# Optimization experiments

Hardware: AMD Instinct MI355X
Metric: run time of the kernel (lower is better)

Reference implementation:

```python
import jax, jax.numpy as jnp
import numpy as np

B, H, V, W = 64, 4, 128000, 200  # batch, heads, vocab, repetition window
N = B * H
NEG = jnp.float32(-1e30)


def setup_inputs() -> dict:
    key = jax.random.key(0)
    ks = jax.random.split(key, 6)
    logits = jax.random.normal(ks[0], (B, H, V), jnp.float32) * 4.0
    output_tokens = jax.random.randint(ks[1], (N, W), 0, V)  # pad value would be V
    temperatures = jax.random.uniform(ks[2], (N,), jnp.float32, 0.5, 1.5)
    top_ps = jax.random.uniform(ks[3], (N,), jnp.float32, 0.7, 1.0)
    top_ks = jax.random.randint(ks[4], (N,), 1, 1025).astype(jnp.int32)
    repetition_penalties = jax.random.uniform(ks[5], (N,), jnp.float32, 1.0, 1.3)
    return {
        "logits": logits,
        "output_tokens": output_tokens,
        "temperatures": temperatures,
        "top_ps": top_ps,
        "top_ks": top_ks,
        "repetition_penalties": repetition_penalties,
    }


def reference(logits, output_tokens, temperatures, top_ps, top_ks, repetition_penalties):
    b, h, v = logits.shape
    n = b * h
    lg = logits.reshape(n, v)

    # --- repetition penalty (bincount-based mask, pad id = v is dropped) ---
    rows = jnp.arange(n)[:, None]
    counts = jnp.zeros((n, v + 1), jnp.int32).at[rows, output_tokens].add(1)[:, :v]
    seen = counts > 0
    rp = jnp.where(seen, repetition_penalties[:, None], 1.0)
    lg = jnp.where(lg > 0, lg / rp, lg * rp)

    # --- temperature ---
    lg = lg / temperatures[:, None]

    # --- top-k / top-p (vLLM: ascending sort, mask, scatter back) ---
    idx = jnp.argsort(lg, axis=-1)                       # ascending
    ls = jnp.take_along_axis(lg, idx, axis=-1)
    kth = jnp.take_along_axis(ls, (v - top_ks.astype(jnp.int32))[:, None], axis=-1)
    ls = jnp.where(ls < kth, NEG, ls)                    # top-k mask
    ps = jax.nn.softmax(ls, axis=-1)
    csum = jnp.cumsum(ps, axis=-1)
    pmask = (csum <= 1.0 - top_ps[:, None]).at[:, -1].set(False)
    ls = jnp.where(pmask, NEG, ls)                       # top-p mask
    inv = jnp.argsort(idx, axis=-1)                      # scatter back
    lg = jnp.take_along_axis(ls, inv, axis=-1)

    # --- softmax + multinomial sample (categorical == multinomial(probs, 1)) ---
    probs = jax.nn.softmax(lg, axis=-1)
    ids = jax.random.categorical(jax.random.key(42), lg, axis=-1).reshape(b, h)
    return ids, probs
```

## Files before the change

### kernel.cpp

```cpp
#include <hip/hip_runtime.h>

#define V 128000
#define V4 (V / 4)
#define V4ALL (NROWS * V4)
#define NCHUNK (V / 16)
#define NROWS 256
#define NSLICE 8
#define SL4 (V4 / NSLICE)
#define W 200
#define VW (V / 32)
#define CAP 4096
#define CAPS 2048
#define CAPM 8192
#define TINYF 1.17549435e-38f
#define HIDX(b) ((b) + ((b) >> 5))
#define HSZ 4224

#define WS_CMAX   0u
#define WS_BMAX   4104192u
#define WS_NEED   16777216u

typedef float vfloat4 __attribute__((ext_vector_type(4)));

__device__ __forceinline__ void bar_lds() {
  asm volatile("s_waitcnt lgkmcnt(0)" ::: "memory");
  __builtin_amdgcn_s_barrier();
}

__device__ __forceinline__ unsigned int fkey(float x) {
  unsigned int u = __float_as_uint(x);
  return (u & 0x80000000u) ? ~u : (u | 0x80000000u);
}
__device__ __forceinline__ float ikey(unsigned int k) {
  unsigned int u = (k & 0x80000000u) ? (k & 0x7FFFFFFFu) : ~k;
  return __uint_as_float(u);
}

__device__ __forceinline__ unsigned int tf_bits(unsigned int t) {
  const unsigned int k0 = 0u, k1 = 42u;
  const unsigned int ks2 = k0 ^ k1 ^ 0x1BD11BDAu;
  unsigned int x0 = 0u + k0, x1 = t + k1;
  const unsigned int ksArr[3] = {k0, k1, ks2};
  const int RA[4] = {13, 15, 26, 6};
  const int RB[4] = {17, 29, 16, 24};
#pragma unroll
  for (int i = 0; i < 5; ++i) {
#pragma unroll
    for (int j = 0; j < 4; ++j) {
      int r = (i & 1) ? RB[j] : RA[j];
      x0 += x1;
      x1 = (x1 << r) | (x1 >> (32 - r));
      x1 ^= x0;
    }
    x0 += ksArr[(i + 1) % 3];
    x1 += ksArr[(i + 2) % 3] + (unsigned int)(i + 1);
  }
  return x0 ^ x1;
}

__device__ __forceinline__ float xform(float x, bool seen, float rp, float irp,
                                        float itemp) {
  if (seen) x = (x > 0.0f) ? x * irp : x * rp;
  return x * itemp;
}

__device__ __forceinline__ void wave_suffix_select_p(const int* hist, int need,
                                                     int lane, int* out_b,
                                                     int* out_rem) {
  int sm = 0;
  const int bb = lane * 64;
  for (int i = 0; i < 64; ++i) sm += hist[HIDX(bb + i)];
  int sfx = sm;
#pragma unroll
  for (int d = 1; d < 64; d <<= 1) {
    int t = __shfl_down(sfx, d);
    if (lane + d < 64) sfx += t;
  }
  unsigned long long mk = __ballot(sfx >= need);
  const int cstar = 63 - __builtin_clzll(mk);
  const int aboveC = __shfl(sfx, cstar) - __shfl(sm, cstar);
  int h = hist[HIDX(cstar * 64 + lane)];
  int sfx2 = h;
#pragma unroll
  for (int d = 1; d < 64; d <<= 1) {
    int t = __shfl_down(sfx2, d);
    if (lane + d < 64) sfx2 += t;
  }
  unsigned long long mk2 = __ballot(aboveC + sfx2 >= need);
  const int boff = 63 - __builtin_clzll(mk2);
  const int aboveB = aboveC + __shfl(sfx2, boff) - __shfl(h, boff);
  if (lane == 0) {
    *out_b = cstar * 64 + boff;
    *out_rem = need - aboveB;
  }
}

__global__ __launch_bounds__(256) void kF_zero(float* __restrict__ probs) {
  vfloat4* __restrict__ p4 = reinterpret_cast<vfloat4*>(probs);
  const vfloat4 z4 = (vfloat4){0.0f, 0.0f, 0.0f, 0.0f};
  const int stride = gridDim.x * 256;
  for (int q = blockIdx.x * 256 + threadIdx.x; q < V4ALL; q += stride)
    p4[q] = z4;
}

__global__ __launch_bounds__(256) void kA_chunkmax(
    const float* __restrict__ logits, const int* __restrict__ toks,
    const float* __restrict__ temps, const float* __restrict__ rps,
    unsigned short* __restrict__ ws_cmax, float* __restrict__ ws_bmax) {
  __shared__ unsigned int s_seen[VW];
  __shared__ float s_red[4];
  const int row = blockIdx.x >> 3;
  const int slice = blockIdx.x & 7;
  const int tid = threadIdx.x;
  const int lane = tid & 63;
  const int wid = tid >> 6;
  const float rp = rps[row];
  const float irp = 1.0f / rp;
  const float itemp = 1.0f / temps[row];
  const size_t base = (size_t)row * V;
  const float4* __restrict__ lg4 = reinterpret_cast<const float4*>(logits + base);

  for (int i = tid; i < VW; i += 256) s_seen[i] = 0u;
  __syncthreads();
  for (int i = tid; i < W; i += 256) {
    int tok = toks[row * W + i];
    if (tok >= 0 && tok < V) atomicOr(&s_seen[tok >> 5], 1u << (tok & 31));
  }
  __syncthreads();

  float lmax = -INFINITY;
  const int q0 = slice * SL4;
  for (int qi = tid; qi < SL4; qi += 256) {
    const int q = q0 + qi;
    float4 x4 = lg4[q];
    float xs[4] = {x4.x, x4.y, x4.z, x4.w};
    const int j0 = q * 4;
    const int sh = j0 & 31;
    unsigned long long ww = (unsigned long long)s_seen[j0 >> 5] |
                            ((unsigned long long)s_seen[(j0 + 3) >> 5] << 32);
    unsigned int kmax = 0u;
#pragma unroll
    for (int e = 0; e < 4; ++e) {
      float x = xform(xs[e], (ww >> (sh + e)) & 1ull, rp, irp, itemp);
      lmax = fmaxf(lmax, x);
      unsigned int ky = fkey(x);
      kmax = kmax > ky ? kmax : ky;
    }
    unsigned int o;
    o = __shfl_xor(kmax, 1); kmax = kmax > o ? kmax : o;
    o = __shfl_xor(kmax, 2); kmax = kmax > o ? kmax : o;
    if ((lane & 3) == 0) ws_cmax[row * NCHUNK + (q >> 2)] = (unsigned short)(kmax >> 16);
  }
#pragma unroll
  for (int d = 32; d > 0; d >>= 1) lmax = fmaxf(lmax, __shfl_xor(lmax, d));
  if (lane == 0) s_red[wid] = lmax;
  __syncthreads();
  if (tid == 0) {
    float mm = fmaxf(fmaxf(s_red[0], s_red[1]), fmaxf(s_red[2], s_red[3]));
    ws_bmax[row * NSLICE + slice] = mm;
  }
}

__global__ __launch_bounds__(1024) void kB_select(
    const float* __restrict__ logits, const int* __restrict__ toks,
    const float* __restrict__ temps, const float* __restrict__ topps,
    const int* __restrict__ topks, const float* __restrict__ rps,
    const unsigned short* __restrict__ ws_cmax, const float* __restrict__ ws_bmax,
    float* __restrict__ out_ids, float* __restrict__ probs) {
  __shared__ unsigned long long s_key[CAP];
  __shared__ __align__(16) unsigned char s_bufA[HSZ*4];
  __shared__ __align__(16) unsigned char s_bufB[16384];
  __shared__ float s_wredf[16];
  __shared__ int s_wredi[16];
  __shared__ float s_mv, s_dn1, s_dn2;
  __shared__ int s_b0, s_cnt, s_scnt, s_selb, s_selrem, s_p0v, s_maxpop;

  int* s_hist0 = (int*)s_key;
  unsigned int* s_seen = (unsigned int*)s_bufA;
  int* s_hist = (int*)s_bufA;
  unsigned short* s_cmax16 = (unsigned short*)s_bufB;
  unsigned long long* s_key2 = (unsigned long long*)s_bufB;
  unsigned long long* s_skey = s_key;
  float* s_e2 = (float*)(s_key + CAPS);
  float* s_q2 = (float*)(s_key + CAPS + CAPS / 2);
  unsigned char* s_keep = (unsigned char*)s_bufA;

  const int row = blockIdx.x;
  const int tid = threadIdx.x;
  const int lane = tid & 63;
  const int wid = tid >> 6;
  const float rp = rps[row];
  const float irp = 1.0f / rp;
  const float itemp = 1.0f / temps[row];
  const float topp = topps[row];
  const int k = topks[row];
  const size_t base = (size_t)row * V;
  const float4* __restrict__ lg4 = reinterpret_cast<const float4*>(logits + base);
  float* __restrict__ prow = probs + base;

  for (int i = tid; i < VW; i += 1024) s_seen[i] = 0u;
  for (int i = tid; i < HSZ; i += 1024) s_hist0[i] = 0;
  {
    const unsigned int* cm32 = reinterpret_cast<const unsigned int*>(ws_cmax + row * NCHUNK);
    unsigned int* sc32 = reinterpret_cast<unsigned int*>(s_cmax16);
    for (int i = tid; i < NCHUNK / 2; i += 1024) sc32[i] = cm32[i];
  }
  __syncthreads();
  for (int i = tid; i < W; i += 1024) {
    int tok = toks[row * W + i];
    if (tok >= 0 && tok < V) atomicOr(&s_seen[tok >> 5], 1u << (tok & 31));
  }
  for (int i = tid; i < NCHUNK; i += 1024)
    atomicAdd(&s_hist0[HIDX(s_cmax16[i] >> 4)], 1);
  __syncthreads();

  if (wid == 1 && lane == 0) {
    float mm = ws_bmax[row * NSLICE];
    for (int i = 1; i < NSLICE; ++i) mm = fmaxf(mm, ws_bmax[row * NSLICE + i]);
    s_mv = mm;
  }
  if (wid == 0) {
    wave_suffix_select_p(s_hist0, k, lane, &s_b0, &s_selrem);
    if (lane == 0) s_cnt = 0;
  }
  __syncthreads();
  const int b0 = s_b0;

  const unsigned int fk0 = ((unsigned int)b0) << 20;
  const int c16 = b0 << 4;
  for (int qb = 0; qb < V4; qb += 1024) {
    const int q = qb + tid;
    const bool act = (q < V4) && ((int)s_cmax16[q >> 2] >= c16);
    unsigned int ks[4];
    bool pr[4] = {false, false, false, false};
    const int j0 = q * 4;
    if (act) {
      float4 x4 = lg4[q];
      float raw[4] = {x4.x, x4.y, x4.z, x4.w};
      const int sh = j0 & 31;
      unsigned long long ww = (unsigned long long)s_seen[j0 >> 5] |
                              ((unsigned long long)s_seen[(j0 + 3) >> 5] << 32);
#pragma unroll
      for (int e = 0; e < 4; ++e) {
        float x = xform(raw[e], (ww >> (sh + e)) & 1ull, rp, irp, itemp);
        ks[e] = fkey(x);
        pr[e] = (ks[e] >= fk0);
      }
    }
    int cnt = (int)pr[0] + (int)pr[1] + (int)pr[2] + (int)pr[3];
    int inc = cnt;
#pragma unroll
    for (int d = 1; d < 64; d <<= 1) {
      int t = __shfl_up(inc, d);
      if (lane >= d) inc += t;
    }
    const int total = __shfl(inc, 63);
    if (total) {
      int basep = 0;
      if (lane == 0) basep = atomicAdd(&s_cnt, total);
      basep = __shfl(basep, 0);
      int off = basep + inc - cnt;
#pragma unroll
      for (int e = 0; e < 4; ++e) {
        if (pr[e]) {
          if (off < CAP)
            s_key[off] = ((unsigned long long)ks[e] << 32) | (unsigned int)(j0 + e);
          ++off;
        }
      }
    }
  }
  bar_lds();
  int G = s_cnt;
  if (G > CAP) G = CAP;
  const int kk = k > G ? G : k;

  for (int i = tid; i < HSZ; i += 1024) s_hist[i] = 0;
  bar_lds();
  for (int i = tid; i < G; i += 1024)
    atomicAdd(&s_hist[HIDX((unsigned int)(s_key[i] >> 52))], 1);
  bar_lds();
  if (wid == 0) {
    wave_suffix_select_p(s_hist, kk, lane, &s_selb, &s_selrem);
    if (lane == 0) s_scnt = 0;
  }
  bar_lds();
  const unsigned int b1 = (unsigned int)s_selb;

  for (int ib = 0; ib < G; ib += 1024) {
    const int i = ib + tid;
    const bool p = (i < G) && ((unsigned int)(s_key[i] >> 52) >= b1);
    unsigned long long mask = __ballot(p);
    if (!mask) continue;
    int basep = 0;
    if (lane == 0) basep = atomicAdd(&s_scnt, __popcll(mask));
    basep = __shfl(basep, 0);
    if (p) {
      int pos = basep + __popcll(mask & ((1ull << lane) - 1ull));
      if (pos < CAPS) s_key2[pos] = s_key[i];
    }
  }
  bar_lds();
  int S = s_scnt;
  if (S > CAPS) S = CAPS;
  const float m = s_mv;

  const unsigned int cbase = b1 << 20;
  const unsigned int span = fkey(m) - cbase;
  int shiftb;
  {
    int bits = 32 - __clz((int)(span | 1u));
    shiftb = bits > 12 ? bits - 12 : 0;
  }
  for (int i = tid; i < HSZ; i += 1024) s_hist[i] = 0;
  bar_lds();
  for (int i = tid; i < S; i += 1024) {
    unsigned int hi = (unsigned int)(s_key2[i] >> 32);
    int b = (int)((hi - cbase) >> shiftb);
    if (b > 4095) b = 4095;
    atomicAdd(&s_hist[HIDX(b)], 1);
  }
  bar_lds();
  if (wid == 0) {
    int T = 0, mx = 0;
    const int bb = lane * 64;
    for (int i = 0; i < 64; ++i) {
      int c = s_hist[HIDX(bb + i)];
      T += c;
      mx = c > mx ? c : mx;
    }
    int ex = T;
#pragma unroll
    for (int d = 1; d < 64; d <<= 1) {
      int t = __shfl_up(ex, d);
      if (lane >= d) ex += t;
    }
    ex -= T;
    int run = ex;
    for (int i = 0; i < 64; ++i) {
      int idx = HIDX(bb + i);
      int c = s_hist[idx];
      s_hist[idx] = run;
      run += c;
    }
#pragma unroll
    for (int d = 32; d > 0; d >>= 1) {
      int o = __shfl_xor(mx, d);
      mx = o > mx ? o : mx;
    }
    if (lane == 0) s_maxpop = mx;
  }
  bar_lds();

  if (s_maxpop <= 16) {
    for (int i = tid; i < S; i += 1024) {
      unsigned long long key = s_key2[i];
      unsigned int hi = (unsigned int)(key >> 32);
      int b = (int)((hi - cbase) >> shiftb);
      if (b > 4095) b = 4095;
      int pos = atomicAdd(&s_hist[HIDX(b)], 1);
      s_skey[pos] = key;
    }
    bar_lds();
    for (int b = tid; b < 4096; b += 1024) {
      int endb = s_hist[HIDX(b)];
      int st = (b == 0) ? 0 : s_hist[HIDX(b - 1)];
      for (int i = st + 1; i < endb; ++i) {
        unsigned long long key = s_skey[i];
        int j = i - 1;
        while (j >= st && s_skey[j] > key) {
          s_skey[j + 1] = s_skey[j];
          --j;
        }
        s_skey[j + 1] = key;
      }
    }
    bar_lds();
  } else {
    int np2 = 2;
    while (np2 < S) np2 <<= 1;
    for (int i = S + tid; i < np2; i += 1024) s_key2[i] = ~0ull;
    bar_lds();
    for (int size = 2; size <= np2; size <<= 1) {
      for (int stride = size >> 1; stride > 0; stride >>= 1) {
        for (int t2 = tid; t2 < (np2 >> 1); t2 += 1024) {
          int pos = 2 * t2 - (t2 & (stride - 1));
          int qq = pos + stride;
          bool up = ((pos & size) == 0);
          unsigned long long a = s_key2[pos], b = s_key2[qq];
          if ((a > b) == up) { s_key2[pos] = b; s_key2[qq] = a; }
        }
        bar_lds();
      }
    }
    for (int i = tid; i < S; i += 1024) s_skey[i] = s_key2[i];
    bar_lds();
  }

  const unsigned int kthkey32 = (unsigned int)(s_skey[S - kk] >> 32);
  for (int i = tid; i < S; i += 1024) {
    unsigned int hi = (unsigned int)(s_skey[i] >> 32);
    if (hi >= kthkey32 && (i == 0 || (unsigned int)(s_skey[i - 1] >> 32) < kthkey32))
      s_p0v = i;
  }
  bar_lds();
  const int p0 = s_p0v;
  const int L = S - p0;

  float part = 0.0f;
  for (int i = tid; i < L; i += 1024) {
    float x = ikey((unsigned int)(s_skey[p0 + i] >> 32));
    float e = expf(x - m);
    s_e2[i] = e;
    part += e;
  }
#pragma unroll
  for (int d = 32; d > 0; d >>= 1) part += __shfl_xor(part, d);
  if (lane == 0) s_wredf[wid] = part;
  bar_lds();
  if (tid == 0) {
    float s = 0.0f;
    for (int i = 0; i < 16; ++i) s += s_wredf[i];
    s_dn1 = s;
  }
  bar_lds();
  const float denom = s_dn1;

  for (int i = tid; i < L; i += 1024) s_q2[i] = s_e2[i] / denom;
  bar_lds();

  if (tid == 0) {
    const float cut = 1.0f - topp;
    float cs = 0.0f;
    int i = 0;
    for (; i + 16 <= L; i += 16) {
      vfloat4 a = *(const vfloat4*)&s_q2[i];
      vfloat4 b = *(const vfloat4*)&s_q2[i + 4];
      vfloat4 c = *(const vfloat4*)&s_q2[i + 8];
      vfloat4 d = *(const vfloat4*)&s_q2[i + 12];
      unsigned int w0, w1, w2, w3;
      cs += a.x; w0  = (cs <= cut) ? 0u : 1u;
      cs += a.y; w0 |= ((cs <= cut) ? 0u : 1u) << 8;
      cs += a.z; w0 |= ((cs <= cut) ? 0u : 1u) << 16;
      cs += a.w; w0 |= ((cs <= cut) ? 0u : 1u) << 24;
      cs += b.x; w1  = (cs <= cut) ? 0u : 1u;
      cs += b.y; w1 |= ((cs <= cut) ? 0u : 1u) << 8;
      cs += b.z; w1 |= ((cs <= cut) ? 0u : 1u) << 16;
      cs += b.w; w1 |= ((cs <= cut) ? 0u : 1u) << 24;
      cs += c.x; w2  = (cs <= cut) ? 0u : 1u;
      cs += c.y; w2 |= ((cs <= cut) ? 0u : 1u) << 8;
      cs += c.z; w2 |= ((cs <= cut) ? 0u : 1u) << 16;
      cs += c.w; w2 |= ((cs <= cut) ? 0u : 1u) << 24;
      cs += d.x; w3  = (cs <= cut) ? 0u : 1u;
      cs += d.y; w3 |= ((cs <= cut) ? 0u : 1u) << 8;
      cs += d.z; w3 |= ((cs <= cut) ? 0u : 1u) << 16;
      cs += d.w; w3 |= ((cs <= cut) ? 0u : 1u) << 24;
      *(unsigned int*)&s_keep[i] = w0;
      *(unsigned int*)&s_keep[i + 4] = w1;
      *(unsigned int*)&s_keep[i + 8] = w2;
      *(unsigned int*)&s_keep[i + 12] = w3;
    }
    for (; i < L; ++i) {
      cs += s_q2[i];
      s_keep[i] = (cs <= cut) ? 0 : 1;
    }
    s_keep[L - 1] = 1;
  }
  bar_lds();

  part = 0.0f;
  for (int i = tid; i < L; i += 1024)
    if (s_keep[i]) part += s_e2[i];
#pragma unroll
  for (int d = 32; d > 0; d >>= 1) part += __shfl_xor(part, d);
  if (lane == 0) s_wredf[wid] = part;
  bar_lds();
  if (tid == 0) {
    float s = 0.0f;
    for (int i = 0; i < 16; ++i) s += s_wredf[i];
    s_dn2 = s;
  }
  bar_lds();
  const float denom2 = s_dn2;

  for (int i = tid; i < L; i += 1024)
    s_e2[i] = s_keep[i] ? (s_e2[i] / denom2) : 0.0f;
  bar_lds();

  float bs = -INFINITY;
  int bi = 0x7FFFFFFF;
  for (int i = tid; i < L; i += 1024) {
    if (!s_keep[i]) continue;
    unsigned long long kv = s_skey[p0 + i];
    int j = (int)(kv & 0xFFFFFFFFull);
    float x = ikey((unsigned int)(kv >> 32));
    unsigned int t = (unsigned int)(row * V) + (unsigned int)j;
    unsigned int bb = tf_bits(t);
    float u = __uint_as_float((bb >> 9) | 0x3f800000u) - 1.0f;
    if (u < TINYF) u = TINYF;
    float g = -logf(-logf(u));
    float sc = x + g;
    if (sc > bs || (sc == bs && j < bi)) { bs = sc; bi = j; }
  }

  for (int i = tid; i < L; i += 1024) {
    int j = (int)(s_skey[p0 + i] & 0xFFFFFFFFull);
    prow[j] = s_e2[i];
  }

#pragma unroll
  for (int d = 32; d > 0; d >>= 1) {
    float ov = __shfl_down(bs, d);
    int oi = __shfl_down(bi, d);
    if (ov > bs || (ov == bs && oi < bi)) { bs = ov; bi = oi; }
  }
  if (lane == 0) { s_wredf[wid] = bs; s_wredi[wid] = bi; }
  bar_lds();
  if (tid == 0) {
    float bb = s_wredf[0];
    int bj = s_wredi[0];
    for (int i = 1; i < 16; ++i) {
      if (s_wredf[i] > bb || (s_wredf[i] == bb && s_wredi[i] < bj)) {
        bb = s_wredf[i];
        bj = s_wredi[i];
      }
    }
    out_ids[row] = (float)bj;
  }
}

__global__ __launch_bounds__(1024, 1) void sampler_mono(
    const float* __restrict__ logits, const int* __restrict__ toks,
    const float* __restrict__ temps, const float* __restrict__ topps,
    const int* __restrict__ topks, const float* __restrict__ rps,
    float* __restrict__ out_ids, float* __restrict__ probs) {
  __shared__ unsigned int s_seen[VW];
  __shared__ int s_hist[4096];
  __shared__ unsigned short s_cmax16[NCHUNK];
  __shared__ float s_sval[CAPM];
  __shared__ int s_sidx[CAPM];
  __shared__ float s_e[CAPM];
  __shared__ unsigned char s_keep[CAPM];
  __shared__ float s_wredf[16];
  __shared__ int s_wredi[16];
  __shared__ float s_m, s_denom, s_denom2;
  __shared__ int s_b0, s_cnt, s_p0;

  const int row = blockIdx.x;
  const int tid = threadIdx.x;
  const int lane = tid & 63;
  const int wid = tid >> 6;
  const float rp = rps[row];
  const float irp = 1.0f / rp;
  const float itemp = 1.0f / temps[row];
  const float topp = topps[row];
  const int k = topks[row];
  const size_t base = (size_t)row * V;
  const float4* __restrict__ lg4 = reinterpret_cast<const float4*>(logits + base);
  vfloat4* __restrict__ pr4 = reinterpret_cast<vfloat4*>(probs + base);

  for (int i = tid; i < VW; i += 1024) s_seen[i] = 0u;
  for (int i = tid; i < 4096; i += 1024) s_hist[i] = 0;
  __syncthreads();
  for (int i = tid; i < W; i += 1024) {
    int tok = toks[row * W + i];
    if (tok >= 0 && tok < V) atomicOr(&s_seen[tok >> 5], 1u << (tok & 31));
  }
  __syncthreads();

  float lmax = -INFINITY;
  for (int qb = 0; qb < V4; qb += 1024) {
    const int q = qb + tid;
    unsigned int kmax = 0u;
    if (q < V4) {
      float4 x4 = lg4[q];
      float xs[4] = {x4.x, x4.y, x4.z, x4.w};
      const int j0 = q * 4;
      const int sh = j0 & 31;
      unsigned long long ww = (unsigned long long)s_seen[j0 >> 5] |
                              ((unsigned long long)s_seen[(j0 + 3) >> 5] << 32);
#pragma unroll
      for (int e = 0; e < 4; ++e) {
        float x = xform(xs[e], (ww >> (sh + e)) & 1ull, rp, irp, itemp);
        lmax = fmaxf(lmax, x);
        unsigned int ky = fkey(x);
        kmax = kmax > ky ? kmax : ky;
      }
    }
    unsigned int o;
    o = __shfl_xor(kmax, 1); kmax = kmax > o ? kmax : o;
    o = __shfl_xor(kmax, 2); kmax = kmax > o ? kmax : o;
    if (((lane & 3) == 0) && (q < V4)) s_cmax16[q >> 2] = (unsigned short)(kmax >> 16);
  }
#pragma unroll
  for (int d = 32; d > 0; d >>= 1) lmax = fmaxf(lmax, __shfl_xor(lmax, d));
  if (lane == 0) s_wredf[wid] = lmax;
  __syncthreads();
  for (int i = tid; i < NCHUNK; i += 1024)
    atomicAdd(&s_hist[s_cmax16[i] >> 4], 1);
  __syncthreads();
  if (wid == 1 && lane == 0) {
    float mm = s_wredf[0];
    for (int i = 1; i < 16; ++i) mm = fmaxf(mm, s_wredf[i]);
    s_m = mm;
  }
  if (wid == 0) {
    int sm = 0;
    const int bb = lane * 64;
    for (int i = 0; i < 64; ++i) sm += s_hist[bb + i];
    int sfx = sm;
#pragma unroll
    for (int d = 1; d < 64; d <<= 1) {
      int t = __shfl_down(sfx, d);
      if (lane + d < 64) sfx += t;
    }
    unsigned long long mk = __ballot(sfx >= k);
    const int cstar = 63 - __builtin_clzll(mk);
    const int above = __shfl(sfx, cstar) - __shfl(sm, cstar);
    int h = s_hist[cstar * 64 + lane];
    int sfx2 = h;
#pragma unroll
    for (int d = 1; d < 64; d <<= 1) {
      int t = __shfl_down(sfx2, d);
      if (lane + d < 64) sfx2 += t;
    }
    unsigned long long mk2 = __ballot(above + sfx2 >= k);
    const int boff = 63 - __builtin_clzll(mk2);
    if (lane == 0) { s_b0 = cstar * 64 + boff; s_cnt = 0; }
  }
  __syncthreads();
  const int b0 = s_b0;
  const unsigned int fk0 = ((unsigned int)b0) << 20;
  const int c16 = b0 << 4;
  for (int qb = 0; qb < V4; qb += 1024) {
    const int q = qb + tid;
    const bool act = (q < V4) && ((int)s_cmax16[q >> 2] >= c16);
    float xs[4];
    bool pr[4] = {false, false, false, false};
    const int j0 = q * 4;
    if (act) {
      float4 x4 = lg4[q];
      float raw[4] = {x4.x, x4.y, x4.z, x4.w};
      const int sh = j0 & 31;
      unsigned long long ww = (unsigned long long)s_seen[j0 >> 5] |
                              ((unsigned long long)s_seen[(j0 + 3) >> 5] << 32);
#pragma unroll
      for (int e = 0; e < 4; ++e) {
        xs[e] = xform(raw[e], (ww >> (sh + e)) & 1ull, rp, irp, itemp);
        pr[e] = (fkey(xs[e]) >= fk0);
      }
    }
#pragma unroll
    for (int e = 0; e < 4; ++e) {
      unsigned long long mask = __ballot(pr[e]);
      if (!mask) continue;
      int basep = 0;
      if (lane == 0) basep = atomicAdd(&s_cnt, __popcll(mask));
      basep = __shfl(basep, 0);
      if (pr[e]) {
        int pos = basep + __popcll(mask & ((1ull << lane) - 1ull));
        if (pos < CAPM) { s_sval[pos] = xs[e]; s_sidx[pos] = j0 + e; }
      }
    }
  }
  __syncthreads();
  int G = s_cnt;
  if (G > CAPM) G = CAPM;
  int np2 = 2;
  while (np2 < G) np2 <<= 1;
  for (int i = G + tid; i < np2; i += 1024) {
    s_sval[i] = INFINITY;
    s_sidx[i] = 0x7FFFFFFF;
  }
  __syncthreads();
  for (int size = 2; size <= np2; size <<= 1) {
    for (int stride = size >> 1; stride > 0; stride >>= 1) {
      for (int t2 = tid; t2 < (np2 >> 1); t2 += 1024) {
        int pos = 2 * t2 - (t2 & (stride - 1));
        int qq = pos + stride;
        bool up = ((pos & size) == 0);
        float v1 = s_sval[pos], v2 = s_sval[qq];
        int i1 = s_sidx[pos], i2 = s_sidx[qq];
        bool gt = (v1 > v2) || (v1 == v2 && i1 > i2);
        if (gt == up) {
          s_sval[pos] = v2; s_sval[qq] = v1;
          s_sidx[pos] = i2; s_sidx[qq] = i1;
        }
      }
      __syncthreads();
    }
  }
  const int kk = k > G ? G : k;
  const float kth = s_sval[G - kk];
  const float m = s_m;
  for (int i = tid; i < G; i += 1024) {
    if (s_sval[i] >= kth && (i == 0 || s_sval[i - 1] < kth)) s_p0 = i;
  }
  __syncthreads();
  const int p0 = s_p0;
  float part = 0.0f;
  for (int i = p0 + tid; i < G; i += 1024) {
    float e = expf(s_sval[i] - m);
    s_e[i] = e;
    part += e;
  }
#pragma unroll
  for (int d = 32; d > 0; d >>= 1) part += __shfl_xor(part, d);
  if (lane == 0) s_wredf[wid] = part;
  __syncthreads();
  if (tid == 0) {
    float s = 0.0f;
    for (int i = 0; i < 16; ++i) s += s_wredf[i];
    s_denom = s;
  }
  __syncthreads();
  const float denom = s_denom;
  if (tid == 0) {
    const float cut = 1.0f - topp;
    float cs = 0.0f;
    for (int i = p0; i < G; ++i) {
      cs += s_e[i] / denom;
      s_keep[i] = (cs <= cut) ? 0 : 1;
    }
    s_keep[G - 1] = 1;
  }
  __syncthreads();
  part = 0.0f;
  for (int i = p0 + tid; i < G; i += 1024)
    if (s_keep[i]) part += s_e[i];
#pragma unroll
  for (int d = 32; d > 0; d >>= 1) part += __shfl_xor(part, d);
  if (lane == 0) s_wredf[wid] = part;
  __syncthreads();
  if (tid == 0) {
    float s = 0.0f;
    for (int i = 0; i < 16; ++i) s += s_wredf[i];
    s_denom2 = s;
  }
  __syncthreads();
  const float denom2 = s_denom2;
  for (int i = p0 + tid; i < G; i += 1024)
    s_e[i] = s_keep[i] ? (s_e[i] / denom2) : 0.0f;
  __syncthreads();
  float bs = -INFINITY;
  int bi = 0x7FFFFFFF;
  for (int i = p0 + tid; i < G; i += 1024) {
    if (!s_keep[i]) continue;
    int j = s_sidx[i];
    unsigned int t = (unsigned int)(row * V) + (unsigned int)j;
    unsigned int bb = tf_bits(t);
    float u = __uint_as_float((bb >> 9) | 0x3f800000u) - 1.0f;
    if (u < TINYF) u = TINYF;
    float g = -logf(-logf(u));
    float sc = s_sval[i] + g;
    if (sc > bs || (sc == bs && j < bi)) { bs = sc; bi = j; }
  }
  const unsigned int kkey = fkey(kth);
  const int k16 = (int)(kkey >> 16);
  for (int q = tid; q < V4; q += 1024) {
    vfloat4 o = (vfloat4){0.0f, 0.0f, 0.0f, 0.0f};
    if ((int)s_cmax16[q >> 2] >= k16) {
      float4 x4 = lg4[q];
      float raw[4] = {x4.x, x4.y, x4.z, x4.w};
      float os[4];
      const int j0 = q * 4;
      const int sh = j0 & 31;
      unsigned long long ww = (unsigned long long)s_seen[j0 >> 5] |
                              ((unsigned long long)s_seen[(j0 + 3) >> 5] << 32);
#pragma unroll
      for (int e = 0; e < 4; ++e) {
        float x = xform(raw[e], (ww >> (sh + e)) & 1ull, rp, irp, itemp);
        float pr = 0.0f;
        if (x >= kth) {
          int j = j0 + e;
          int lo = p0, hi = G;
          while (lo < hi) {
            int mid = (lo + hi) >> 1;
            float v = s_sval[mid];
            int id = s_sidx[mid];
            if (v < x || (v == x && id < j)) lo = mid + 1; else hi = mid;
          }
          pr = s_e[lo];
        }
        os[e] = pr;
      }
      o.x = os[0]; o.y = os[1]; o.z = os[2]; o.w = os[3];
    }
    pr4[q] = o;
  }
#pragma unroll
  for (int d = 32; d > 0; d >>= 1) {
    float ov = __shfl_down(bs, d);
    int oi = __shfl_down(bi, d);
    if (ov > bs || (ov == bs && oi < bi)) { bs = ov; bi = oi; }
  }
  if (lane == 0) { s_wredf[wid] = bs; s_wredi[wid] = bi; }
  __syncthreads();
  if (tid == 0) {
    float bb = s_wredf[0];
    int bj = s_wredi[0];
    for (int i = 1; i < 16; ++i) {
      if (s_wredf[i] > bb || (s_wredf[i] == bb && s_wredi[i] < bj)) {
        bb = s_wredf[i];
        bj = s_wredi[i];
      }
    }
    out_ids[row] = (float)bj;
  }
}

extern "C" void kernel_launch(void* const* d_in, const int* in_sizes, int n_in,
                              void* d_out, int out_size, void* d_ws, size_t ws_size,
                              hipStream_t stream) {
  (void)in_sizes; (void)out_size;
  if (n_in < 6) return;
  const float* logits = (const float*)d_in[0];
  const int* toks = (const int*)d_in[1];
  const float* temps = (const float*)d_in[2];
  const float* topps = (const float*)d_in[3];
  const int* topks = (const int*)d_in[4];
  const float* rps = (const float*)d_in[5];
  float* out = (float*)d_out;
  float* probs = out + NROWS;

  if (ws_size >= WS_NEED && d_ws != nullptr) {
    char* w = (char*)d_ws;
    unsigned short* ws_cmax = (unsigned short*)(w + WS_CMAX);
    float* ws_bmax = (float*)(w + WS_BMAX);
    kF_zero<<<dim3(2048), dim3(256), 0, stream>>>(probs);
    kA_chunkmax<<<dim3(NROWS * NSLICE), dim3(256), 0, stream>>>(
        logits, toks, temps, rps, ws_cmax, ws_bmax);
    kB_select<<<dim3(NROWS), dim3(1024), 0, stream>>>(
        logits, toks, temps, topps, topks, rps, ws_cmax, ws_bmax, out, probs);
  } else {
    sampler_mono<<<dim3(NROWS), dim3(1024), 0, stream>>>(
        logits, toks, temps, topps, topks, rps, out, probs);
  }
}
```

Baseline: 119.7 us.

## Split select kernel into threshold, sliced gather, and finish kernels

Breaks the per-row 1024-thread select kernel into three kernels. A small kernel computes the coarse threshold bucket from the chunk maxima. A gather kernel with 8 blocks per row then scans logit slices in parallel and appends candidate keys to global workspace through a global atomic counter. A finish kernel loads those keys and runs the remaining selection and sampling. Histograms are also replicated four ways in LDS to reduce atomic contention. The aim is more parallelism in the logit-scanning pass, at the cost of extra launches and global round-trips for keys and counters.

```diff
diff --git a/kernel.cpp b/kernel.cpp
--- a/kernel.cpp
+++ b/kernel.cpp
@@ -2,11 +2,12 @@
 
 #define V 128000
 #define V4 (V / 4)
+#define NROWS 256
 #define V4ALL (NROWS * V4)
 #define NCHUNK (V / 16)
-#define NROWS 256
 #define NSLICE 8
 #define SL4 (V4 / NSLICE)
+#define SLC (NCHUNK / NSLICE)
 #define W 200
 #define VW (V / 32)
 #define CAP 4096
@@ -18,6 +19,9 @@
 
 #define WS_CMAX   0u
 #define WS_BMAX   4104192u
+#define WS_B0     4112384u
+#define WS_CNT    4113408u
+#define WS_KEYS   8388608u
 #define WS_NEED   16777216u
 
 typedef float vfloat4 __attribute__((ext_vector_type(4)));
@@ -161,79 +165,73 @@
   }
 }
 
-__global__ __launch_bounds__(1024) void kB_select(
-    const float* __restrict__ logits, const int* __restrict__ toks,
-    const float* __restrict__ temps, const float* __restrict__ topps,
-    const int* __restrict__ topks, const float* __restrict__ rps,
-    const unsigned short* __restrict__ ws_cmax, const float* __restrict__ ws_bmax,
-    float* __restrict__ out_ids, float* __restrict__ probs) {
-  __shared__ unsigned long long s_key[CAP];
-  __shared__ __align__(16) unsigned char s_bufA[HSZ*4];
-  __shared__ __align__(16) unsigned char s_bufB[16384];
-  __shared__ float s_wredf[16];
-  __shared__ int s_wredi[16];
-  __shared__ float s_mv, s_dn1, s_dn2;
-  __shared__ int s_b0, s_cnt, s_scnt, s_selb, s_selrem, s_p0v, s_maxpop;
-
-  int* s_hist0 = (int*)s_key;
-  unsigned int* s_seen = (unsigned int*)s_bufA;
-  int* s_hist = (int*)s_bufA;
-  unsigned short* s_cmax16 = (unsigned short*)s_bufB;
-  unsigned long long* s_key2 = (unsigned long long*)s_bufB;
-  unsigned long long* s_skey = s_key;
-  float* s_e2 = (float*)(s_key + CAPS);
-  float* s_q2 = (float*)(s_key + CAPS + CAPS / 2);
-  unsigned char* s_keep = (unsigned char*)s_bufA;
-
+__global__ __launch_bounds__(1024) void kS_b0(
+    const unsigned short* __restrict__ ws_cmax, const int* __restrict__ topks,
+    int* __restrict__ ws_b0, int* __restrict__ ws_cnt) {
+  __shared__ int s_h[4 * HSZ];
+  __shared__ int s_b, s_rem;
   const int row = blockIdx.x;
   const int tid = threadIdx.x;
   const int lane = tid & 63;
   const int wid = tid >> 6;
+  for (int i = tid; i < 4 * HSZ; i += 1024) s_h[i] = 0;
+  __syncthreads();
+  const unsigned short* cm = ws_cmax + row * NCHUNK;
+  const int rep = (tid & 3) * HSZ;
+  for (int i = tid; i < NCHUNK; i += 1024)
+    atomicAdd(&s_h[rep + HIDX(cm[i] >> 4)], 1);
+  __syncthreads();
+  for (int i = tid; i < HSZ; i += 1024)
+    s_h[i] += s_h[i + HSZ] + s_h[i + 2 * HSZ] + s_h[i + 3 * HSZ];
+  __syncthreads();
+  if (wid == 0) wave_suffix_select_p(s_h, topks[row], lane, &s_b, &s_rem);
+  __syncthreads();
+  if (tid == 0) {
+    ws_b0[row] = s_b;
+    ws_cnt[row] = 0;
+  }
+}
+
+__global__ __launch_bounds__(256) void kB1_gather(
+    const float* __restrict__ logits, const int* __restrict__ toks,
+    const float* __restrict__ temps, const float* __restrict__ rps,
+    const unsigned short* __restrict__ ws_cmax, const int* __restrict__ ws_b0,
+    int* __restrict__ ws_cnt, unsigned long long* __restrict__ ws_keys) {
+  __shared__ unsigned int s_seen[VW];
+  __shared__ unsigned short s_cm[SLC];
+  const int row = blockIdx.x >> 3;
+  const int slice = blockIdx.x & 7;
+  const int tid = threadIdx.x;
+  const int lane = tid & 63;
   const float rp = rps[row];
   const float irp = 1.0f / rp;
   const float itemp = 1.0f / temps[row];
-  const float topp = topps[row];
-  const int k = topks[row];
   const size_t base = (size_t)row * V;
   const float4* __restrict__ lg4 = reinterpret_cast<const float4*>(logits + base);
-  float* __restrict__ prow = probs + base;
-
-  for (int i = tid; i < VW; i += 1024) s_seen[i] = 0u;
-  for (int i = tid; i < HSZ; i += 1024) s_hist0[i] = 0;
-  {
-    const unsigned int* cm32 = reinterpret_cast<const unsigned int*>(ws_cmax + row * NCHUNK);
-    unsigned int* sc32 = reinterpret_cast<unsigned int*>(s_cmax16);
-    for (int i = tid; i < NCHUNK / 2; i += 1024) sc32[i] = cm32[i];
-  }
-  __syncthreads();
-  for (int i = tid; i < W; i += 1024) {
+
+  for (int i = tid; i < VW; i += 256) s_seen[i] = 0u;
+  for (int i = tid; i < SLC; i += 256)
+    s_cm[i] = ws_cmax[row * NCHUNK + slice * SLC + i];
+  __syncthreads();
+  for (int i = tid; i < W; i += 256) {
     int tok = toks[row * W + i];
     if (tok >= 0 && tok < V) atomicOr(&s_seen[tok >> 5], 1u << (tok & 31));
   }
-  for (int i = tid; i < NCHUNK; i += 1024)
-    atomicAdd(&s_hist0[HIDX(s_cmax16[i] >> 4)], 1);
-  __syncthreads();
-
-  if (wid == 1 && lane == 0) {
-    float mm = ws_bmax[row * NSLICE];
-    for (int i = 1; i < NSLICE; ++i) mm = fmaxf(mm, ws_bmax[row * NSLICE + i]);
-    s_mv = mm;
-  }
-  if (wid == 0) {
-    wave_suffix_select_p(s_hist0, k, lane, &s_b0, &s_selrem);
-    if (lane == 0) s_cnt = 0;
-  }
-  __syncthreads();
-  const int b0 = s_b0;
-
+  __syncthreads();
+
+  const int b0 = ws_b0[row];
   const unsigned int fk0 = ((unsigned int)b0) << 20;
   const int c16 = b0 << 4;
-  for (int qb = 0; qb < V4; qb += 1024) {
-    const int q = qb + tid;
-    const bool act = (q < V4) && ((int)s_cmax16[q >> 2] >= c16);
+  unsigned long long* __restrict__ krow = ws_keys + (size_t)row * CAP;
+  const int q0 = slice * SL4;
+  for (int qb = 0; qb < SL4; qb += 256) {
+    const int qi = qb + tid;
+    const bool inb = (qi < SL4);
+    const bool act = inb && ((int)s_cm[qi >> 2] >= c16);
+    const int q = q0 + qi;
+    const int j0 = q * 4;
     unsigned int ks[4];
     bool pr[4] = {false, false, false, false};
-    const int j0 = q * 4;
     if (act) {
       float4 x4 = lg4[q];
       float raw[4] = {x4.x, x4.y, x4.z, x4.w};
@@ -257,31 +255,72 @@
     const int total = __shfl(inc, 63);
     if (total) {
       int basep = 0;
-      if (lane == 0) basep = atomicAdd(&s_cnt, total);
+      if (lane == 0) basep = atomicAdd(&ws_cnt[row], total);
       basep = __shfl(basep, 0);
       int off = basep + inc - cnt;
 #pragma unroll
       for (int e = 0; e < 4; ++e) {
         if (pr[e]) {
           if (off < CAP)
-            s_key[off] = ((unsigned long long)ks[e] << 32) | (unsigned int)(j0 + e);
+            krow[off] = ((unsigned long long)ks[e] << 32) | (unsigned int)(j0 + e);
           ++off;
         }
       }
     }
   }
-  bar_lds();
-  int G = s_cnt;
+}
+
+__global__ __launch_bounds__(1024) void kB2_finish(
+    const float* __restrict__ topps, const int* __restrict__ topks,
+    const float* __restrict__ ws_bmax, const int* __restrict__ ws_cnt,
+    const unsigned long long* __restrict__ ws_keys,
+    float* __restrict__ out_ids, float* __restrict__ probs) {
+  __shared__ unsigned long long s_key[CAP];
+  __shared__ __align__(16) int s_h[4 * HSZ];
+  __shared__ __align__(16) unsigned char s_bufB[16384];
+  __shared__ float s_wredf[16];
+  __shared__ int s_wredi[16];
+  __shared__ float s_mv, s_dn1, s_dn2;
+  __shared__ int s_scnt, s_selb, s_selrem, s_p0v, s_maxpop;
+
+  unsigned long long* s_key2 = (unsigned long long*)s_bufB;
+  unsigned long long* s_skey = s_key;
+  float* s_e2 = (float*)(s_key + CAPS);
+  float* s_q2 = (float*)(s_key + CAPS + CAPS / 2);
+  unsigned char* s_keep = (unsigned char*)s_h;
+
+  const int row = blockIdx.x;
+  const int tid = threadIdx.x;
+  const int lane = tid & 63;
+  const int wid = tid >> 6;
+  const float topp = topps[row];
+  const int k = topks[row];
+  float* __restrict__ prow = probs + (size_t)row * V;
+
+  int G = ws_cnt[row];
   if (G > CAP) G = CAP;
   const int kk = k > G ? G : k;
-
-  for (int i = tid; i < HSZ; i += 1024) s_hist[i] = 0;
-  bar_lds();
+  {
+    const unsigned long long* krow = ws_keys + (size_t)row * CAP;
+    for (int i = tid; i < G; i += 1024) s_key[i] = krow[i];
+  }
+  if (wid == 1 && lane == 0) {
+    float mm = ws_bmax[row * NSLICE];
+    for (int i = 1; i < NSLICE; ++i) mm = fmaxf(mm, ws_bmax[row * NSLICE + i]);
+    s_mv = mm;
+  }
+  for (int i = tid; i < 4 * HSZ; i += 1024) s_h[i] = 0;
+  __syncthreads();
+
+  const int rep = (tid & 3) * HSZ;
   for (int i = tid; i < G; i += 1024)
-    atomicAdd(&s_hist[HIDX((unsigned int)(s_key[i] >> 52))], 1);
+    atomicAdd(&s_h[rep + HIDX((unsigned int)(s_key[i] >> 52))], 1);
+  bar_lds();
+  for (int i = tid; i < HSZ; i += 1024)
+    s_h[i] += s_h[i + HSZ] + s_h[i + 2 * HSZ] + s_h[i + 3 * HSZ];
   bar_lds();
   if (wid == 0) {
-    wave_suffix_select_p(s_hist, kk, lane, &s_selb, &s_selrem);
+    wave_suffix_select_p(s_h, kk, lane, &s_selb, &s_selrem);
     if (lane == 0) s_scnt = 0;
   }
   bar_lds();
@@ -312,20 +351,23 @@
     int bits = 32 - __clz((int)(span | 1u));
     shiftb = bits > 12 ? bits - 12 : 0;
   }
-  for (int i = tid; i < HSZ; i += 1024) s_hist[i] = 0;
+  for (int i = tid; i < 4 * HSZ; i += 1024) s_h[i] = 0;
   bar_lds();
   for (int i = tid; i < S; i += 1024) {
     unsigned int hi = (unsigned int)(s_key2[i] >> 32);
     int b = (int)((hi - cbase) >> shiftb);
     if (b > 4095) b = 4095;
-    atomicAdd(&s_hist[HIDX(b)], 1);
-  }
+    atomicAdd(&s_h[rep + HIDX(b)], 1);
+  }
+  bar_lds();
+  for (int i = tid; i < HSZ; i += 1024)
+    s_h[i] += s_h[i + HSZ] + s_h[i + 2 * HSZ] + s_h[i + 3 * HSZ];
   bar_lds();
   if (wid == 0) {
     int T = 0, mx = 0;
     const int bb = lane * 64;
     for (int i = 0; i < 64; ++i) {
-      int c = s_hist[HIDX(bb + i)];
+      int c = s_h[HIDX(bb + i)];
       T += c;
       mx = c > mx ? c : mx;
     }
@@ -339,8 +381,8 @@
     int run = ex;
     for (int i = 0; i < 64; ++i) {
       int idx = HIDX(bb + i);
-      int c = s_hist[idx];
-      s_hist[idx] = run;
+      int c = s_h[idx];
+      s_h[idx] = run;
       run += c;
     }
 #pragma unroll
@@ -358,13 +400,13 @@
       unsigned int hi = (unsigned int)(key >> 32);
       int b = (int)((hi - cbase) >> shiftb);
       if (b > 4095) b = 4095;
-      int pos = atomicAdd(&s_hist[HIDX(b)], 1);
+      int pos = atomicAdd(&s_h[HIDX(b)], 1);
       s_skey[pos] = key;
     }
     bar_lds();
     for (int b = tid; b < 4096; b += 1024) {
-      int endb = s_hist[HIDX(b)];
-      int st = (b == 0) ? 0 : s_hist[HIDX(b - 1)];
+      int endb = s_h[HIDX(b)];
+      int st = (b == 0) ? 0 : s_h[HIDX(b - 1)];
       for (int i = st + 1; i < endb; ++i) {
         unsigned long long key = s_skey[i];
         int j = i - 1;
@@ -827,11 +869,17 @@
     char* w = (char*)d_ws;
     unsigned short* ws_cmax = (unsigned short*)(w + WS_CMAX);
     float* ws_bmax = (float*)(w + WS_BMAX);
+    int* ws_b0 = (int*)(w + WS_B0);
+    int* ws_cnt = (int*)(w + WS_CNT);
+    unsigned long long* ws_keys = (unsigned long long*)(w + WS_KEYS);
     kF_zero<<<dim3(2048), dim3(256), 0, stream>>>(probs);
     kA_chunkmax<<<dim3(NROWS * NSLICE), dim3(256), 0, stream>>>(
         logits, toks, temps, rps, ws_cmax, ws_bmax);
-    kB_select<<<dim3(NROWS), dim3(1024), 0, stream>>>(
-        logits, toks, temps, topps, topks, rps, ws_cmax, ws_bmax, out, probs);
+    kS_b0<<<dim3(NROWS), dim3(1024), 0, stream>>>(ws_cmax, topks, ws_b0, ws_cnt);
+    kB1_gather<<<dim3(NROWS * NSLICE), dim3(256), 0, stream>>>(
+        logits, toks, temps, rps, ws_cmax, ws_b0, ws_cnt, ws_keys);
+    kB2_finish<<<dim3(NROWS), dim3(1024), 0, stream>>>(
+        topps, topks, ws_bmax, ws_cnt, ws_keys, out, probs);
   } else {
     sampler_mono<<<dim3(NROWS), dim3(1024), 0, stream>>>(
         logits, toks, temps, topps, topks, rps, out, probs);
```

After: 205.6 us. +71.8%, slower.
